# Kernel tuning notes

Measured on AMD Instinct MI355X. Metric: run time of the kernel, lower is better.

## Reference

```python
import jax, jax.numpy as jnp
import numpy as np

B = 65536  # number of 32-bit words processed by the VM


def _build_tables():
    # ByteToNibbleFFN: byte one-hot -> (high, low) nibble one-hots
    W1_b2n = np.eye(256, dtype=np.float32)
    W2_b2n = np.zeros((256, 32), dtype=np.float32)
    for b in range(256):
        W2_b2n[b, (b >> 4) & 15] = 1.0
        W2_b2n[b, 16 + (b & 15)] = 1.0
    # NibbleToByteFFN: (high, low) -> byte one-hot
    W1_n2b = np.zeros((32, 256), dtype=np.float32)
    for high in range(16):
        for low in range(16):
            bv = (high << 4) | low
            W1_n2b[high, bv] = 1.0
            W1_n2b[16 + low, bv] = 1.0
    W2_n2b = np.eye(256, dtype=np.float32)
    # NibbleTableFFN for XOR
    W1_xor = np.zeros((32, 256), dtype=np.float32)
    W2_xor = np.zeros((256, 16), dtype=np.float32)
    for a in range(16):
        for b in range(16):
            k = a * 16 + b
            W1_xor[a, k] = 1.0
            W1_xor[16 + b, k] = 1.0
            W2_xor[k, (a ^ b) & 15] = 1.0
    # NibbleAddFFN: (a, b, carry) -> (sum, carry)
    W1_add = np.zeros((34, 512), dtype=np.float32)
    W2_sum = np.zeros((512, 16), dtype=np.float32)
    W2_carry = np.zeros((512, 2), dtype=np.float32)
    for a in range(16):
        for b in range(16):
            for c in range(2):
                k = a * 32 + b * 2 + c
                W1_add[a, k] = 1.0
                W1_add[16 + b, k] = 1.0
                W1_add[32 + c, k] = 1.0
                total = a + b + c
                W2_sum[k, total & 15] = 1.0
                W2_carry[k, 1 if total >= 16 else 0] = 1.0
    return (jnp.asarray(W1_b2n), jnp.asarray(W2_b2n), jnp.asarray(W1_n2b),
            jnp.asarray(W2_n2b), jnp.asarray(W1_xor), jnp.asarray(W2_xor),
            jnp.asarray(W1_add), jnp.asarray(W2_sum), jnp.asarray(W2_carry))


def setup_inputs() -> dict:
    key = jax.random.key(0)
    k1, k2 = jax.random.split(key)
    a_idx = jax.random.randint(k1, (B, 4), 0, 256)
    b_idx = jax.random.randint(k2, (B, 4), 0, 256)
    a_bytes = jax.nn.one_hot(a_idx, 256, dtype=jnp.float32)  # [B,4,256]
    b_bytes = jax.nn.one_hot(b_idx, 256, dtype=jnp.float32)
    (W1_b2n, W2_b2n, W1_n2b, W2_n2b, W1_xor, W2_xor,
     W1_add, W2_sum, W2_carry) = _build_tables()
    return {
        'a_bytes': a_bytes, 'b_bytes': b_bytes,
        'W1_b2n': W1_b2n, 'W2_b2n': W2_b2n,
        'W1_n2b': W1_n2b, 'W2_n2b': W2_n2b,
        'W1_xor': W1_xor, 'W2_xor': W2_xor,
        'W1_add': W1_add, 'W2_sum': W2_sum, 'W2_carry': W2_carry,
    }


def reference(a_bytes, b_bytes, W1_b2n, W2_b2n, W1_n2b, W2_n2b,
              W1_xor, W2_xor, W1_add, W2_sum, W2_carry):
    # Batched faithful translation of the torch VM: the torch code loops over
    # single words; here each op is vectorized over the word batch B while the
    # fixed 4-byte carry chain remains an explicit (structural) loop.
    def byte_to_nib(x):                       # x: [B,256]
        w = jax.nn.softmax((x @ W1_b2n) * 100.0, axis=-1)
        nib = w @ W2_b2n                      # [B,32]
        return nib[:, :16], nib[:, 16:]

    def nib_to_byte(high, low):               # [B,16] each -> [B,256]
        x = jnp.concatenate([high, low], axis=-1)
        w = jax.nn.softmax((x @ W1_n2b - 1.5) * 20.0, axis=-1)
        return w @ W2_n2b

    def nib_xor(a, b):                        # [B,16] each -> [B,16]
        x = jnp.concatenate([a, b], axis=-1)
        w = jax.nn.softmax((x @ W1_xor - 1.5) * 20.0, axis=-1)
        return w @ W2_xor

    def nib_add(a, b, c):                     # [B,16],[B,16],[B,2]
        x = jnp.concatenate([a, b, c], axis=-1)
        w = jax.nn.softmax((x @ W1_add - 2.5) * 20.0, axis=-1)
        return w @ W2_sum, w @ W2_carry

    def byte_xor(a, b):                       # [B,256] each
        a_h, a_l = byte_to_nib(a)
        b_h, b_l = byte_to_nib(b)
        return nib_to_byte(nib_xor(a_h, b_h), nib_xor(a_l, b_l))

    n = a_bytes.shape[0]
    # ByteAddFFN: 4-byte ripple-carry add, carry starts as one-hot 0
    carry = jnp.broadcast_to(jnp.array([1.0, 0.0], dtype=a_bytes.dtype), (n, 2))
    sum_bytes = []
    for i in range(4):
        a_h, a_l = byte_to_nib(a_bytes[:, i])
        b_h, b_l = byte_to_nib(b_bytes[:, i])
        r_low, carry_low = nib_add(a_l, b_l, carry)
        r_high, carry = nib_add(a_h, b_h, carry_low)
        sum_bytes.append(nib_to_byte(r_high, r_low))
    # Chain a second VM op: XOR the sum with operand a, per byte
    out = [byte_xor(sum_bytes[i], a_bytes[:, i]) for i in range(4)]
    return jnp.stack(out, axis=1)             # [B,4,256]
```

## Files before the change

### kernel.cpp

```cpp
#include <hip/hip_runtime.h>
#include <stdint.h>

typedef float f32x4 __attribute__((ext_vector_type(4)));
typedef float f32x2 __attribute__((ext_vector_type(2)));


__global__ __launch_bounds__(256) void vm_phase1(
    const float* __restrict__ a_bytes,
    const float* __restrict__ b_bytes,
    uint32_t* __restrict__ ws,
    int n_words)
{
    const int lane = threadIdx.x & 63;
    const int w    = blockIdx.x * 4 + (threadIdx.x >> 6);
    if (w >= n_words) return;

    const float* pa = a_bytes + (long)w * 1024;
    const float* pb = b_bytes + (long)w * 1024;

    f32x2 v[8];
#pragma unroll
    for (int c = 0; c < 8; ++c) {
        const float* p = (c < 4 ? pa + c * 256 : pb + (c - 4) * 256) + lane * 2;
        v[c] = __builtin_nontemporal_load((const f32x2*)p);
    }

    uint32_t idx[8];
    bool found[8];
#pragma unroll
    for (int c = 0; c < 8; ++c) {
        const uint64_t m0 = __ballot(v[c].x > 0.5f);
        const uint64_t m1 = __ballot(v[c].y > 0.5f);
        const uint64_t m  = m0 | m1;
        found[c] = (m != 0);
        idx[c] = 2u * ((uint32_t)__ffsll((unsigned long long)m) - 1u) +
                 (m1 ? 1u : 0u);
    }

#pragma unroll
    for (int c = 0; c < 8; ++c) {
        if (!found[c]) {
            const float* p = (c < 4 ? pa + c * 256 : pb + (c - 4) * 256) + 128 + lane * 2;
            v[c] = __builtin_nontemporal_load((const f32x2*)p);
        }
    }
#pragma unroll
    for (int c = 0; c < 8; ++c) {
        if (!found[c]) {
            const uint64_t m0 = __ballot(v[c].x > 0.5f);
            const uint64_t m1 = __ballot(v[c].y > 0.5f);
            const uint64_t m  = m0 | m1;
            idx[c] = 128u + 2u * ((uint32_t)__ffsll((unsigned long long)m) - 1u) +
                     (m1 ? 1u : 0u);
        }
    }

    const uint32_t aw = idx[0] | (idx[1] << 8) | (idx[2] << 16) | (idx[3] << 24);
    const uint32_t bw = idx[4] | (idx[5] << 8) | (idx[6] << 16) | (idx[7] << 24);
    const uint32_t s = aw + bw;
    const uint32_t o = s ^ aw;
    if (lane == 0) ws[w] = o;
}

__global__ __launch_bounds__(256) void vm_phase2(
    const uint32_t* __restrict__ ws,
    float* __restrict__ out,
    int n_words)
{
    const int lane = threadIdx.x & 63;
    const int w    = blockIdx.x * 4 + (threadIdx.x >> 6);
    if (w >= n_words) return;

    const uint32_t o = ws[w];
    float* po = out + (long)w * 1024 + lane * 4;
    const int j = lane * 4;
#pragma unroll
    for (int k = 0; k < 4; ++k) {
        const int oi = (int)((o >> (8 * k)) & 255u);
        f32x4 ov;
        ov.x = (j     == oi) ? 1.0f : 0.0f;
        ov.y = (j + 1 == oi) ? 1.0f : 0.0f;
        ov.z = (j + 2 == oi) ? 1.0f : 0.0f;
        ov.w = (j + 3 == oi) ? 1.0f : 0.0f;
        *(f32x4*)(po + k * 256) = ov;
    }
}

__device__ __forceinline__ uint32_t idx_of16(const f32x4 v) {
    const uint64_t m0 = __ballot(v.x > 0.5f);
    const uint64_t m1 = __ballot(v.y > 0.5f);
    const uint64_t m2 = __ballot(v.z > 0.5f);
    const uint64_t m3 = __ballot(v.w > 0.5f);
    const uint64_t m  = m0 | m1 | m2 | m3;
    const uint32_t hl = (uint32_t)__ffsll((unsigned long long)m) - 1u;
    const uint32_t c  = (m1 ? 1u : 0u) | (m2 ? 2u : 0u) | (m3 ? 3u : 0u);
    return hl * 4u + c;
}

__global__ __launch_bounds__(256) void vm_fused(
    const float* __restrict__ a_bytes,
    const float* __restrict__ b_bytes,
    float* __restrict__ out,
    int n_words)
{
    const int lane = threadIdx.x & 63;
    const int w    = blockIdx.x * 4 + (threadIdx.x >> 6);
    if (w >= n_words) return;

    const long base = (long)w * 1024 + lane * 4;
    const float* pa = a_bytes + base;
    const float* pb = b_bytes + base;

    const f32x4 a0 = __builtin_nontemporal_load((const f32x4*)(pa));
    const f32x4 a1 = __builtin_nontemporal_load((const f32x4*)(pa + 256));
    const f32x4 a2 = __builtin_nontemporal_load((const f32x4*)(pa + 512));
    const f32x4 a3 = __builtin_nontemporal_load((const f32x4*)(pa + 768));
    const f32x4 b0 = __builtin_nontemporal_load((const f32x4*)(pb));
    const f32x4 b1 = __builtin_nontemporal_load((const f32x4*)(pb + 256));
    const f32x4 b2 = __builtin_nontemporal_load((const f32x4*)(pb + 512));
    const f32x4 b3 = __builtin_nontemporal_load((const f32x4*)(pb + 768));

    const uint32_t aw = idx_of16(a0) | (idx_of16(a1) << 8) |
                        (idx_of16(a2) << 16) | (idx_of16(a3) << 24);
    const uint32_t bw = idx_of16(b0) | (idx_of16(b1) << 8) |
                        (idx_of16(b2) << 16) | (idx_of16(b3) << 24);
    const uint32_t s = aw + bw;
    const uint32_t o = s ^ aw;

    float* po = out + base;
    const int j = lane * 4;
#pragma unroll
    for (int k = 0; k < 4; ++k) {
        const int oi = (int)((o >> (8 * k)) & 255u);
        f32x4 ov;
        ov.x = (j     == oi) ? 1.0f : 0.0f;
        ov.y = (j + 1 == oi) ? 1.0f : 0.0f;
        ov.z = (j + 2 == oi) ? 1.0f : 0.0f;
        ov.w = (j + 3 == oi) ? 1.0f : 0.0f;
        __builtin_nontemporal_store(ov, (f32x4*)(po + k * 256));
    }
}

extern "C" void kernel_launch(void* const* d_in, const int* in_sizes, int n_in,
                              void* d_out, int out_size, void* d_ws, size_t ws_size,
                              hipStream_t stream)
{
    const float* a_bytes = (const float*)d_in[0];
    const float* b_bytes = (const float*)d_in[1];
    float* out = (float*)d_out;
    const int n_words = in_sizes[0] / 1024;
    const int blocks  = (n_words + 3) / 4;

    if (d_ws != nullptr && ws_size >= (size_t)n_words * 4) {
        uint32_t* ws = (uint32_t*)d_ws;
        vm_phase1<<<blocks, 256, 0, stream>>>(a_bytes, b_bytes, ws, n_words);
        vm_phase2<<<blocks, 256, 0, stream>>>(ws, out, n_words);
    } else {
        vm_fused<<<blocks, 256, 0, stream>>>(a_bytes, b_bytes, out, n_words);
    }
}
```

Before: 548.0 us.

## Probe one-hot bytes via 16-bit high-half loads with iterative early exit

Phase 1 now reads only 16-bit halves of the one-hot floats and compares them against the bf16 pattern of 1.0 (0x3F80). Each wave scans a 256-float row in 32-element chunks and stops as soon as every row's hot index is found. The aim is to cut the read traffic spent on locating the single hot entry. In exchange it issues narrow 2-byte loads, each 128-byte window in its own round. Rounds are serialized by a dependent loop, so latency may dominate, and 32-byte memory sectors mean half of each fetched sector is wasted.

Measured after the change: 646.9 us. +18.0%, slower.

```diff
diff --git a/kernel.cpp b/kernel.cpp
--- a/kernel.cpp
+++ b/kernel.cpp
@@ -2,7 +2,6 @@
 #include <stdint.h>
 
 typedef float f32x4 __attribute__((ext_vector_type(4)));
-typedef float f32x2 __attribute__((ext_vector_type(2)));
 
 
 __global__ __launch_bounds__(256) void vm_phase1(
@@ -15,43 +14,48 @@
     const int w    = blockIdx.x * 4 + (threadIdx.x >> 6);
     if (w >= n_words) return;
 
-    const float* pa = a_bytes + (long)w * 1024;
-    const float* pb = b_bytes + (long)w * 1024;
+    const unsigned short* pa = (const unsigned short*)(a_bytes + (long)w * 1024);
+    const unsigned short* pb = (const unsigned short*)(b_bytes + (long)w * 1024);
 
-    f32x2 v[8];
-#pragma unroll
-    for (int c = 0; c < 8; ++c) {
-        const float* p = (c < 4 ? pa + c * 256 : pb + (c - 4) * 256) + lane * 2;
-        v[c] = __builtin_nontemporal_load((const f32x2*)p);
-    }
-
+    unsigned short val[8];
     uint32_t idx[8];
     bool found[8];
-#pragma unroll
-    for (int c = 0; c < 8; ++c) {
-        const uint64_t m0 = __ballot(v[c].x > 0.5f);
-        const uint64_t m1 = __ballot(v[c].y > 0.5f);
-        const uint64_t m  = m0 | m1;
-        found[c] = (m != 0);
-        idx[c] = 2u * ((uint32_t)__ffsll((unsigned long long)m) - 1u) +
-                 (m1 ? 1u : 0u);
-    }
 
 #pragma unroll
     for (int c = 0; c < 8; ++c) {
-        if (!found[c]) {
-            const float* p = (c < 4 ? pa + c * 256 : pb + (c - 4) * 256) + 128 + lane * 2;
-            v[c] = __builtin_nontemporal_load((const f32x2*)p);
-        }
+        const unsigned short* p =
+            (c < 4 ? pa + c * 512 : pb + (c - 4) * 512) + lane;
+        val[c] = __builtin_nontemporal_load(p);
     }
 #pragma unroll
     for (int c = 0; c < 8; ++c) {
-        if (!found[c]) {
-            const uint64_t m0 = __ballot(v[c].x > 0.5f);
-            const uint64_t m1 = __ballot(v[c].y > 0.5f);
-            const uint64_t m  = m0 | m1;
-            idx[c] = 128u + 2u * ((uint32_t)__ffsll((unsigned long long)m) - 1u) +
-                     (m1 ? 1u : 0u);
+        const uint64_t m = __ballot(val[c] == (unsigned short)0x3F80);
+        found[c] = (m != 0);
+        idx[c] = (((uint32_t)__ffsll((unsigned long long)m)) - 1u) >> 1;
+    }
+
+    for (int r = 1; r < 8; ++r) {
+        bool all = found[0] & found[1] & found[2] & found[3] &
+                   found[4] & found[5] & found[6] & found[7];
+        if (all) break;
+#pragma unroll
+        for (int c = 0; c < 8; ++c) {
+            if (!found[c]) {
+                const unsigned short* p =
+                    (c < 4 ? pa + c * 512 : pb + (c - 4) * 512) + r * 64 + lane;
+                val[c] = __builtin_nontemporal_load(p);
+            }
+        }
+#pragma unroll
+        for (int c = 0; c < 8; ++c) {
+            if (!found[c]) {
+                const uint64_t m = __ballot(val[c] == (unsigned short)0x3F80);
+                if (m != 0) {
+                    found[c] = true;
+                    idx[c] = (uint32_t)r * 32u +
+                             ((((uint32_t)__ffsll((unsigned long long)m)) - 1u) >> 1);
+                }
+            }
         }
     }
 
```
